# Kernel optimization log

Measured on AMD Instinct MI355X. Metric: run time of the kernel, lower is better.

## Reference

```python
import jax, jax.numpy as jnp
import numpy as np

IN_DIM, UNITS, OUT_DIM = 128, 256, 8
DENSITY = 0.5  # 1 - sparsity_level
B, T = 256, 512


def _ncp_dims():
    Nm = OUT_DIM
    Nc = max(int(0.4 * (UNITS - Nm)), 1)   # command neurons (AutoNCP rule)
    Ni = UNITS - Nm - Nc                    # inter neurons
    return Ni, Nc, Nm


def _fanout_mask(rng, n_src, n_dst, fanout):
    # each source connects to `fanout` distinct random destinations
    idx = np.argsort(rng.random((n_src, n_dst)), axis=1)[:, :fanout]
    m = np.zeros((n_src, n_dst), dtype=np.int32)
    m[np.arange(n_src)[:, None], idx] = 1
    return m


def setup_inputs() -> dict:
    key = jax.random.key(0)
    rng = np.random.default_rng(22222)
    Ni, Nc, Nm = _ncp_dims()
    s_fan = max(int(Ni * DENSITY), 1)       # sensory fanout
    i_fan = max(int(Nc * DENSITY), 1)       # inter fanout
    m_fanin = max(int(Nc * DENSITY), 1)     # motor fanin
    M_si = _fanout_mask(rng, IN_DIM, Ni, s_fan)      # sensory -> inter
    M_ic = _fanout_mask(rng, Ni, Nc, i_fan)          # inter -> command
    M_cm = _fanout_mask(rng, Nm, Nc, m_fanin).T      # command -> motor (fanin per motor)

    def layer_mask(M_in, hid):
        # WiredCfCCell: concat input sparsity with dense ones for the recurrent block, then transpose
        return np.concatenate([M_in, np.ones((hid, hid), np.int32)], axis=0).T

    masks = [layer_mask(M_si, Ni), layer_mask(M_ic, Nc), layer_mask(M_cm, Nm)]
    dims = [(IN_DIM, Ni), (Ni, Nc), (Nc, Nm)]
    inp = {}
    for l, (fin, hid) in enumerate(dims):
        cat = fin + hid
        scale = 1.0 / np.sqrt(cat)
        for nm in ("w1", "w2", "wa", "wb"):
            inp[f"{nm}_{l}"] = jnp.asarray(rng.normal(0.0, scale, (hid, cat)).astype(np.float32))
        for nm in ("b1", "b2", "ba", "bb"):
            inp[f"{nm}_{l}"] = jnp.zeros((hid,), jnp.float32)
        inp[f"m{l}"] = jnp.asarray(masks[l])  # int32, constant sparsity mask
    k1, k2 = jax.random.split(key)
    inp["x"] = jax.random.normal(k1, (B, T, IN_DIM), jnp.float32)
    inp["dt"] = jax.random.uniform(k2, (1,), jnp.float32, 0.5, 1.5)
    return inp


def _cfc_cell(xh, w1, b1, w2, b2, wa, ba, wb, bb, m, ts):
    # CfCCell, mode='default', no backbone, sparsity mask on ff1/ff2 weights
    mf = m.astype(w1.dtype)
    ff1 = jnp.tanh(xh @ (w1 * mf).T + b1)
    ff2 = jnp.tanh(xh @ (w2 * mf).T + b2)
    t_interp = jax.nn.sigmoid((xh @ wa.T + ba) * ts + (xh @ wb.T + bb))
    return ff1 * (1.0 - t_interp) + t_interp * ff2


def _forward(x, dt, params, masks):
    Ni, Nc, Nm = _ncp_dims()
    ts = dt[0]
    h0 = jnp.zeros((x.shape[0], Ni), x.dtype)
    h1 = jnp.zeros((x.shape[0], Nc), x.dtype)
    h2 = jnp.zeros((x.shape[0], Nm), x.dtype)
    p0, p1, p2 = params

    def step(carry, xt):
        h0, h1, h2 = carry
        nh0 = _cfc_cell(jnp.concatenate([xt, h0], 1), *p0, masks[0], ts)
        nh1 = _cfc_cell(jnp.concatenate([nh0, h1], 1), *p1, masks[1], ts)
        nh2 = _cfc_cell(jnp.concatenate([nh1, h2], 1), *p2, masks[2], ts)
        return (nh0, nh1, nh2), nh2

    (h0, h1, h2), ys = jax.lax.scan(step, (h0, h1, h2), jnp.swapaxes(x, 0, 1))
    y = jnp.tanh(jnp.swapaxes(ys, 0, 1))          # (B, T, OUT_DIM), tanh output saturation
    h_out = jnp.concatenate([h0, h1, h2], axis=1)  # (B, units)
    return y, h_out


def reference(x, dt,
              w1_0, b1_0, w2_0, b2_0, wa_0, ba_0, wb_0, bb_0, m0,
              w1_1, b1_1, w2_1, b2_1, wa_1, ba_1, wb_1, bb_1, m1,
              w1_2, b1_2, w2_2, b2_2, wa_2, ba_2, wb_2, bb_2, m2):
    params = ((w1_0, b1_0, w2_0, b2_0, wa_0, ba_0, wb_0, bb_0),
              (w1_1, b1_1, w2_1, b2_1, wa_1, ba_1, wb_1, bb_1),
              (w1_2, b1_2, w2_2, b2_2, wa_2, ba_2, wb_2, bb_2))
    return _forward(x, dt, params, (m0, m1, m2))
```

## Files before the change

kernel.cpp:

```cpp
#include <hip/hip_runtime.h>
#include <cmath>


typedef _Float16 f16;
typedef f16 h4 __attribute__((ext_vector_type(4)));
typedef f16 h8 __attribute__((ext_vector_type(8)));
typedef float f4 __attribute__((ext_vector_type(4)));

#define MFMA(a, b, c) __builtin_amdgcn_mfma_f32_16x16x32_f16(a, b, c, 0, 0, 0)
#define RAW_BAR() asm volatile("s_waitcnt lgkmcnt(0)\n\ts_barrier" ::: "memory")

constexpr int IN_DIM = 128, Ni = 149, Nc = 99, Nm = 8;
constexpr int CAT0 = 277, CAT1 = 248, CAT2 = 107;
constexpr int Bsz = 256, Tsz = 512;
constexpr int TC = 64, NCH = 8, NBT = 16;
constexpr int NT0 = 30, NT1 = 21;
constexpr int S0 = 168, S2 = 136;
constexpr int NXWG1 = 64;
constexpr int NXWG0 = 128;
constexpr size_t XU0C = (size_t)TC * NBT * NT0 * 256;
constexpr size_t NH0C = (size_t)TC * NBT * 2560;
constexpr size_t XU1C = (size_t)TC * NBT * NT1 * 256;
constexpr size_t H0S_HALVES = (size_t)NBT * 16 * S0;
constexpr size_t H12S_HALVES = (size_t)NBT * 2 * 16 * S2;
constexpr size_t YOFF = (size_t)Bsz * Tsz * 8;
constexpr float L2E = 1.4426950408889634f;

constexpr int OFF_X0 = 0;
constexpr int OFF_R0 = 7680;
constexpr int OFF_X1 = 17280;
constexpr int OFF_R12A = 24000;
constexpr int OFF_R12B = 29376;
constexpr int NFRAG = 30144;

__device__ inline float rcpf_(float x) { return __builtin_amdgcn_rcpf(x); }
__device__ __forceinline__ float exp2p_(float x) {
#if __has_builtin(__builtin_amdgcn_exp2f)
  return __builtin_amdgcn_exp2f(x);
#else
  return exp2f(x);
#endif
}
__device__ __forceinline__ float cfc_h(float a0, float a1, float a2) {
  float e0 = exp2p_(a0), e1 = exp2p_(a1), e2 = exp2p_(a2);
  float pa = 1.f + e0, ma = 1.f - e0;
  float pb = 1.f + e1, mb = 1.f - e1;
  float pc = 1.f + e2;
  float num = fmaf(ma * pb, e2, mb * pa);
  return num * rcpf_(pa * pb * pc);
}
__device__ __forceinline__ float tanhp_(float x) {
  float e = exp2p_(-2.f * L2E * x);
  return (1.f - e) * rcpf_(1.f + e);
}

__global__ __launch_bounds__(256) void pack_kernel(
    const float* __restrict__ w1_0, const float* __restrict__ w2_0,
    const float* __restrict__ wa_0, const float* __restrict__ wb_0,
    const int* __restrict__ m0,
    const float* __restrict__ w1_1, const float* __restrict__ w2_1,
    const float* __restrict__ wa_1, const float* __restrict__ wb_1,
    const int* __restrict__ m1,
    const float* __restrict__ w1_2, const float* __restrict__ w2_2,
    const float* __restrict__ wa_2, const float* __restrict__ wb_2,
    const int* __restrict__ m2, const float* __restrict__ dtp,
    f16* __restrict__ PK, int* __restrict__ CNT) {
  if (blockIdx.x == 0 && threadIdx.x < NCH)
    __hip_atomic_store(&CNT[threadIdx.x], 0, __ATOMIC_RELAXED,
                       __HIP_MEMORY_SCOPE_AGENT);
  int idx = blockIdx.x * 256 + threadIdx.x;
  if (idx >= NFRAG) return;
  int lane = idx & 63, col = lane & 15, q = lane >> 4;
  float ts = dtp[0];
  const float* Wa = nullptr;
  const float* Wb = nullptr;
  const int* M = nullptr;
  int ld, n, nmax, k0, kmax;
  int mat;
  if (idx < OFF_R0) {
    int p = idx >> 6;
    mat = p / 40; int nt = (p >> 2) % 10, kt = p & 3;
    ld = CAT0; n = nt * 16 + col; nmax = Ni; k0 = kt * 32 + q * 8; kmax = IN_DIM;
    if (mat == 0) { Wa = w1_0; M = m0; }
    else if (mat == 1) { Wa = w2_0; M = m0; }
    else { Wa = wa_0; Wb = wb_0; }
  } else if (idx < OFF_X1) {
    int p = (idx - OFF_R0) >> 6;
    int g = p / 15; mat = (p / 5) % 3; int kt = p % 5;
    ld = CAT0; n = g * 16 + col; nmax = Ni; k0 = IN_DIM + kt * 32 + q * 8; kmax = CAT0;
    if (mat == 0) Wa = w1_0;
    else if (mat == 1) Wa = w2_0;
    else { Wa = wa_0; Wb = wb_0; }
  } else if (idx < OFF_R12A) {
    int p = (idx - OFF_X1) >> 6;
    mat = p / 35; int nt = (p / 5) % 7, kt = p % 5;
    ld = CAT1; n = nt * 16 + col; nmax = Nc; k0 = kt * 32 + q * 8; kmax = Ni;
    if (mat == 0) { Wa = w1_1; M = m1; }
    else if (mat == 1) { Wa = w2_1; M = m1; }
    else { Wa = wa_1; Wb = wb_1; }
  } else if (idx < OFF_R12B) {
    int p = (idx - OFF_R12A) >> 6;
    int wv = p / 12; mat = (p / 4) % 3; int kt = p & 3;
    ld = CAT1; n = wv * 16 + col; nmax = Nc; k0 = Ni + kt * 32 + q * 8; kmax = CAT1;
    if (mat == 0) Wa = w1_1;
    else if (mat == 1) Wa = w2_1;
    else { Wa = wa_1; Wb = wb_1; }
  } else {
    int p = (idx - OFF_R12B) >> 6;
    mat = p / 4; int kt = p & 3;
    ld = CAT2; n = col; nmax = Nm; k0 = kt * 32 + q * 8; kmax = CAT2;
    if (mat == 0) { Wa = w1_2; M = m2; }
    else if (mat == 1) { Wa = w2_2; M = m2; }
    else { Wa = wa_2; Wb = wb_2; }
  }
  h8 r;
#pragma unroll
  for (int j = 0; j < 8; j++) {
    int k = k0 + j;
    float v = 0.f;
    if (n < nmax && k < kmax) {
      if (mat < 2) {
        v = Wa[(size_t)n * ld + k];
        if (M) v *= (float)M[(size_t)n * ld + k];
        v *= -2.f * L2E;
      } else {
        v = -L2E * (ts * Wa[(size_t)n * ld + k] + Wb[(size_t)n * ld + k]);
      }
    }
    r[j] = (f16)v;
  }
  ((h8*)PK)[idx] = r;
}

__device__ __forceinline__ void r0_step(
    const f16* br, f16* bw, const f16* __restrict__ XU0, f16* __restrict__ NH0,
    float* __restrict__ out, const h8 (&Bf)[3][5], h4 (&xu)[3],
    int t, int tload, int bt, int g, int lane, int col, int q, int n, bool last) {
  h8 A[5];
#pragma unroll
  for (int kt = 0; kt < 5; kt++)
    A[kt] = *(const h8*)(br + col * S0 + kt * 32 + q * 8);
  f4 acc0 = {(float)xu[0][0], (float)xu[0][1], (float)xu[0][2], (float)xu[0][3]};
  f4 acc1 = {(float)xu[1][0], (float)xu[1][1], (float)xu[1][2], (float)xu[1][3]};
  f4 acc2 = {(float)xu[2][0], (float)xu[2][1], (float)xu[2][2], (float)xu[2][3]};
  size_t mtl = (size_t)tload * NBT + bt;
#pragma unroll
  for (int mat = 0; mat < 3; mat++)
    xu[mat] = *(const h4*)(XU0 + (mtl * NT0 + mat * 10 + g) * 256 + lane * 4);
#pragma unroll
  for (int kt = 0; kt < 5; kt++) {
    acc0 = MFMA(A[kt], Bf[0][kt], acc0);
    acc1 = MFMA(A[kt], Bf[1][kt], acc1);
    acc2 = MFMA(A[kt], Bf[2][kt], acc2);
  }
  int mt = t * NBT + bt;
  f16* nh = NH0 + (size_t)mt * 2560;
#pragma unroll
  for (int r = 0; r < 4; r++) {
    int m = q * 4 + r;
    float h = cfc_h(acc0[r], acc1[r], acc2[r]);
    f16 h16 = (f16)h;
    bw[m * S0 + n] = h16;
    nh[m * 160 + n] = h16;
    if (last && n < Ni) out[YOFF + (size_t)(bt * 16 + m) * 256 + n] = h;
  }
}

__device__ __forceinline__ void r12l1_step(
    const f16* br, f16* bw, const f16* __restrict__ XU1, float* __restrict__ out,
    const h8 (&Bf)[3][4], h4 (&xu)[3],
    int tload, int bt, int w, int lane, int col, int q, int n, bool last) {
  h8 A[4];
#pragma unroll
  for (int kt = 0; kt < 4; kt++)
    A[kt] = *(const h8*)(br + col * S2 + kt * 32 + q * 8);
  f4 acc0 = {(float)xu[0][0], (float)xu[0][1], (float)xu[0][2], (float)xu[0][3]};
  f4 acc1 = {(float)xu[1][0], (float)xu[1][1], (float)xu[1][2], (float)xu[1][3]};
  f4 acc2 = {(float)xu[2][0], (float)xu[2][1], (float)xu[2][2], (float)xu[2][3]};
  size_t mtl = (size_t)tload * NBT + bt;
#pragma unroll
  for (int mat = 0; mat < 3; mat++)
    xu[mat] = *(const h4*)(XU1 + (mtl * NT1 + mat * 7 + w) * 256 + lane * 4);
#pragma unroll
  for (int kt = 0; kt < 4; kt++) {
    acc0 = MFMA(A[kt], Bf[0][kt], acc0);
    acc1 = MFMA(A[kt], Bf[1][kt], acc1);
    acc2 = MFMA(A[kt], Bf[2][kt], acc2);
  }
#pragma unroll
  for (int r = 0; r < 4; r++) {
    int m = q * 4 + r;
    float h = cfc_h(acc0[r], acc1[r], acc2[r]);
    if (n < Nc) {
      bw[m * S2 + n] = (f16)h;
      if (last) out[YOFF + (size_t)(bt * 16 + m) * 256 + Ni + n] = h;
    }
  }
}

__device__ __forceinline__ void r12l2_step(
    const f16* rb, f16* wb, float* __restrict__ out, const h8 (&Bf)[3][4],
    float bn0, float bn1, float bn2, int tg, int bt, int col, int q, bool last) {
  h8 A[4];
#pragma unroll
  for (int kt = 0; kt < 4; kt++)
    A[kt] = *(const h8*)(rb + col * S2 + kt * 32 + q * 8);
  f4 acc0 = {bn0, bn0, bn0, bn0};
  f4 acc1 = {bn1, bn1, bn1, bn1};
  f4 acc2 = {bn2, bn2, bn2, bn2};
#pragma unroll
  for (int kt = 0; kt < 4; kt++) {
    acc0 = MFMA(A[kt], Bf[0][kt], acc0);
    acc1 = MFMA(A[kt], Bf[1][kt], acc1);
    acc2 = MFMA(A[kt], Bf[2][kt], acc2);
  }
#pragma unroll
  for (int r = 0; r < 4; r++) {
    int m = q * 4 + r;
    float h = cfc_h(acc0[r], acc1[r], acc2[r]);
    if (col < Nm) {
      out[((size_t)(bt * 16 + m) * Tsz + tg) * 8 + col] = tanhp_(h);
      wb[m * S2 + Nc + col] = (f16)h;
      if (last) out[YOFF + (size_t)(bt * 16 + m) * 256 + Ni + Nc + col] = h;
    }
  }
}

__global__ __launch_bounds__(640) void R_kernel(
    const h8* __restrict__ pk,
    const float* __restrict__ b1_0, const float* __restrict__ b2_0,
    const float* __restrict__ ba_0, const float* __restrict__ bb_0,
    const float* __restrict__ b1_1, const float* __restrict__ b2_1,
    const float* __restrict__ ba_1, const float* __restrict__ bb_1,
    const float* __restrict__ c1, const float* __restrict__ c2,
    const float* __restrict__ ca, const float* __restrict__ cb,
    const float* __restrict__ dtp, const float* __restrict__ x,
    f16* __restrict__ XU0, f16* __restrict__ NH0, f16* __restrict__ XU1,
    f16* __restrict__ H0S, f16* __restrict__ H12S,
    int* __restrict__ CNT, float* __restrict__ out, int c) {
  __shared__ __align__(16) char smem[10752];
  int tid = threadIdx.x;
  int g = tid >> 6, lane = tid & 63, col = lane & 15, q = lane >> 4;
  int wg = blockIdx.x;
  float ts = dtp[0];

  if (wg < NBT) {
    if (c < 0 || c >= NCH) return;
    const f16* XU0r = XU0 + (size_t)(c & 1) * XU0C;
    f16* NH0w = NH0 + (size_t)(c & 1) * NH0C;
    f16(*buf)[16 * S0] = (f16(*)[16 * S0])smem;
    int bt = wg;
    int n = g * 16 + col;
    h8 Bf[3][5];
#pragma unroll
    for (int mat = 0; mat < 3; mat++)
#pragma unroll
      for (int kt = 0; kt < 5; kt++)
        Bf[mat][kt] = pk[OFF_R0 + ((g * 3 + mat) * 5 + kt) * 64 + lane];

    for (int idx = tid; idx < 16 * S0; idx += 640) {
      buf[0][idx] = (c == 0) ? (f16)0.f : H0S[(size_t)bt * 16 * S0 + idx];
      buf[1][idx] = (f16)0.f;
    }
    __syncthreads();

    h4 xu0[3], xu1[3], xu2[3], xu3[3];
#pragma unroll
    for (int mat = 0; mat < 3; mat++) {
      xu0[mat] = *(const h4*)(XU0r + ((size_t)(0 * NBT + bt) * NT0 + mat * 10 + g) * 256 + lane * 4);
      xu1[mat] = *(const h4*)(XU0r + ((size_t)(1 * NBT + bt) * NT0 + mat * 10 + g) * 256 + lane * 4);
      xu2[mat] = *(const h4*)(XU0r + ((size_t)(2 * NBT + bt) * NT0 + mat * 10 + g) * 256 + lane * 4);
      xu3[mat] = *(const h4*)(XU0r + ((size_t)(3 * NBT + bt) * NT0 + mat * 10 + g) * 256 + lane * 4);
    }

    for (int t = 0; t < TC; t += 4) {
      r0_step(buf[0], buf[1], XU0r, NH0w, out, Bf, xu0, t, (t + 4 < TC) ? t + 4 : t,
              bt, g, lane, col, q, n, false);
      RAW_BAR();
      r0_step(buf[1], buf[0], XU0r, NH0w, out, Bf, xu1, t + 1,
              (t + 5 < TC) ? t + 5 : t + 1, bt, g, lane, col, q, n, false);
      RAW_BAR();
      r0_step(buf[0], buf[1], XU0r, NH0w, out, Bf, xu2, t + 2,
              (t + 6 < TC) ? t + 6 : t + 2, bt, g, lane, col, q, n, false);
      RAW_BAR();
      bool lastD = (c == NCH - 1) && (t + 3 == TC - 1);
      r0_step(buf[1], buf[0], XU0r, NH0w, out, Bf, xu3, t + 3,
              (t + 7 < TC) ? t + 7 : t + 3, bt, g, lane, col, q, n, lastD);
      RAW_BAR();
    }
    for (int idx = tid; idx < 16 * S0; idx += 640)
      H0S[(size_t)bt * 16 * S0 + idx] = buf[0][idx];

  } else if (wg < 2 * NBT) {
    int cc = c - 1;
    if (cc < 0 || cc >= NCH) return;
    const f16* XU1r = XU1 + (size_t)(cc & 1) * XU1C;
    f16(*buf)[16 * S2] = (f16(*)[16 * S2])smem;
    int bt = wg - NBT;
    int w = g;
    int n = w * 16 + col;
    h8 Bf[3][4];
    float bn0 = 0.f, bn1 = 0.f, bn2 = 0.f;
    if (w < 7) {
#pragma unroll
      for (int mat = 0; mat < 3; mat++)
#pragma unroll
        for (int kt = 0; kt < 4; kt++)
          Bf[mat][kt] = pk[OFF_R12A + ((w * 3 + mat) * 4 + kt) * 64 + lane];
    } else if (w == 7) {
#pragma unroll
      for (int mat = 0; mat < 3; mat++)
#pragma unroll
        for (int kt = 0; kt < 4; kt++)
          Bf[mat][kt] = pk[OFF_R12B + (mat * 4 + kt) * 64 + lane];
      bn0 = (col < Nm) ? -2.f * L2E * c1[col] : 0.f;
      bn1 = (col < Nm) ? -2.f * L2E * c2[col] : 0.f;
      bn2 = (col < Nm) ? -L2E * (ts * ca[col] + cb[col]) : 0.f;
    }
    for (int idx = tid; idx < 2 * 16 * S2; idx += 640)
      ((f16*)buf)[idx] = (cc == 0) ? (f16)0.f : H12S[(size_t)bt * 2 * 16 * S2 + idx];
    __syncthreads();

    if (tid == 0) {
      long it = 0;
      while (__hip_atomic_load(&CNT[cc], __ATOMIC_RELAXED,
                               __HIP_MEMORY_SCOPE_AGENT) < NXWG1 &&
             it < (1L << 28)) {
        __builtin_amdgcn_s_sleep(8);
        ++it;
      }
    }
    __syncthreads();
    __builtin_amdgcn_fence(__ATOMIC_ACQUIRE, "agent");

    h4 xuA[3], xuB[3];
    if (w < 7) {
#pragma unroll
      for (int mat = 0; mat < 3; mat++) {
        xuA[mat] = *(const h4*)(XU1r + ((size_t)bt * NT1 + mat * 7 + w) * 256 + lane * 4);
        xuB[mat] = *(const h4*)(XU1r +
                                ((size_t)(NBT + bt) * NT1 + mat * 7 + w) * 256 + lane * 4);
      }
    }

    for (int t = 0; t < TC; t += 2) {
      if (w < 7) {
        int tlA = (t + 2 < TC) ? t + 2 : t;
        r12l1_step(buf[0], buf[1], XU1r, out, Bf, xuA, tlA, bt, w, lane, col, q, n,
                   false);
      }
      RAW_BAR();
      if (w == 7)
        r12l2_step(buf[1], buf[0], out, Bf, bn0, bn1, bn2, cc * TC + t, bt, col, q,
                   false);
      if (w < 7) {
        int tlB = (t + 3 < TC) ? t + 3 : t + 1;
        bool lastB = (cc == NCH - 1) && (t + 1 == TC - 1);
        r12l1_step(buf[1], buf[0], XU1r, out, Bf, xuB, tlB, bt, w, lane, col, q, n,
                   lastB);
      }
      RAW_BAR();
      if (w == 7)
        r12l2_step(buf[0], buf[1], out, Bf, bn0, bn1, bn2, cc * TC + t + 1, bt, col, q,
                   (cc == NCH - 1) && (t + 1 == TC - 1));
    }
    __syncthreads();
    for (int idx = tid; idx < 2 * 16 * S2; idx += 640)
      H12S[(size_t)bt * 2 * 16 * S2 + idx] = ((f16*)buf)[idx];

  } else if (wg < 2 * NBT + NXWG1) {
    int cx = c - 1;
    if (cx < 0 || cx >= NCH) return;
    int w = g;
    const f16* NH0r = NH0 + (size_t)(cx & 1) * NH0C;
    f16* XU1w = XU1 + (size_t)(cx & 1) * XU1C;
    int bx = wg - 2 * NBT;
    int n = w * 16 + col;
    if (w < 7) {
      h8 Bf[3][5];
      float bias[3];
#pragma unroll
      for (int mat = 0; mat < 3; mat++)
#pragma unroll
        for (int kt = 0; kt < 5; kt++)
          Bf[mat][kt] = pk[OFF_X1 + (mat * 35 + w * 5 + kt) * 64 + lane];
      bias[0] = (n < Nc) ? -2.f * L2E * b1_1[n] : 0.f;
      bias[1] = (n < Nc) ? -2.f * L2E * b2_1[n] : 0.f;
      bias[2] = (n < Nc) ? -L2E * (ts * ba_1[n] + bb_1[n]) : 0.f;
      for (int i = 0; i < (TC * NBT) / NXWG1; i++) {
        int mt = bx * ((TC * NBT) / NXWG1) + i;
        const f16* Ab = NH0r + (size_t)mt * 2560;
        h8 A[5];
#pragma unroll
        for (int kt = 0; kt < 5; kt++)
          A[kt] = *(const h8*)(Ab + col * 160 + kt * 32 + q * 8);
#pragma unroll
        for (int mat = 0; mat < 3; mat++) {
          float b = bias[mat];
          f4 acc = {b, b, b, b};
#pragma unroll
          for (int kt = 0; kt < 5; kt++) acc = MFMA(A[kt], Bf[mat][kt], acc);
          h4 o;
#pragma unroll
          for (int rr = 0; rr < 4; rr++) o[rr] = (f16)acc[rr];
          *(h4*)(XU1w + ((size_t)mt * NT1 + mat * 7 + w) * 256 + lane * 4) = o;
        }
      }
    }
    __syncthreads();
    if (tid == 0)
      __hip_atomic_fetch_add(&CNT[cx], 1, __ATOMIC_RELEASE,
                             __HIP_MEMORY_SCOPE_AGENT);

  } else {
    int cn = c + 1;
    if (cn >= NCH) return;
    f16* XU0w = XU0 + (size_t)(cn & 1) * XU0C;
    f16* stg = (f16*)smem;
    int bx = wg - 2 * NBT - NXWG1;
    int w = g;
    int n = w * 16 + col;
    h8 Bx[3][4];
    float bias[3];
#pragma unroll
    for (int mat = 0; mat < 3; mat++)
#pragma unroll
      for (int kt = 0; kt < 4; kt++)
        Bx[mat][kt] = pk[OFF_X0 + ((mat * 10 + w) * 4 + kt) * 64 + lane];
    bias[0] = (n < Ni) ? -2.f * L2E * b1_0[n] : 0.f;
    bias[1] = (n < Ni) ? -2.f * L2E * b2_0[n] : 0.f;
    bias[2] = (n < Ni) ? -L2E * (ts * ba_0[n] + bb_0[n]) : 0.f;
    for (int i = 0; i < (TC * NBT) / NXWG0; i++) {
      int mt = bx * ((TC * NBT) / NXWG0) + i;
      int tl = mt >> 4, bt = mt & 15;
      int tg = cn * TC + tl;
      if (tid < 256) {
        int sr = tid >> 4, sc = (tid & 15) * 8;
        const float* xp = x + ((size_t)(bt * 16 + sr) * Tsz + tg) * IN_DIM + sc;
        h8 hv;
#pragma unroll
        for (int j = 0; j < 8; j++) hv[j] = (f16)xp[j];
        *(h8*)(stg + sr * 136 + sc) = hv;
      }
      __syncthreads();
      h8 A[4];
#pragma unroll
      for (int kt = 0; kt < 4; kt++)
        A[kt] = *(const h8*)(stg + col * 136 + kt * 32 + q * 8);
#pragma unroll
      for (int mat = 0; mat < 3; mat++) {
        float b = bias[mat];
        f4 acc = {b, b, b, b};
#pragma unroll
        for (int kt = 0; kt < 4; kt++) acc = MFMA(A[kt], Bx[mat][kt], acc);
        h4 o;
#pragma unroll
        for (int rr = 0; rr < 4; rr++) o[rr] = (f16)acc[rr];
        *(h4*)(XU0w + ((size_t)mt * NT0 + mat * 10 + w) * 256 + lane * 4) = o;
      }
      __syncthreads();
    }
  }
}

extern "C" void kernel_launch(void* const* d_in, const int* in_sizes, int n_in,
                              void* d_out, int out_size, void* d_ws, size_t ws_size,
                              hipStream_t stream) {
  const float* w1_0 = (const float*)d_in[0];
  const float* w2_0 = (const float*)d_in[1];
  const float* wa_0 = (const float*)d_in[2];
  const float* wb_0 = (const float*)d_in[3];
  const float* b1_0 = (const float*)d_in[4];
  const float* b2_0 = (const float*)d_in[5];
  const float* ba_0 = (const float*)d_in[6];
  const float* bb_0 = (const float*)d_in[7];
  const int* m0 = (const int*)d_in[8];
  const float* w1_1 = (const float*)d_in[9];
  const float* w2_1 = (const float*)d_in[10];
  const float* wa_1 = (const float*)d_in[11];
  const float* wb_1 = (const float*)d_in[12];
  const float* b1_1 = (const float*)d_in[13];
  const float* b2_1 = (const float*)d_in[14];
  const float* ba_1 = (const float*)d_in[15];
  const float* bb_1 = (const float*)d_in[16];
  const int* m1 = (const int*)d_in[17];
  const float* w1_2 = (const float*)d_in[18];
  const float* w2_2 = (const float*)d_in[19];
  const float* wa_2 = (const float*)d_in[20];
  const float* wb_2 = (const float*)d_in[21];
  const float* c1 = (const float*)d_in[22];
  const float* c2 = (const float*)d_in[23];
  const float* ca = (const float*)d_in[24];
  const float* cb = (const float*)d_in[25];
  const int* m2 = (const int*)d_in[26];
  const float* x = (const float*)d_in[27];
  const float* dt = (const float*)d_in[28];
  float* out = (float*)d_out;

  f16* XU0 = (f16*)d_ws;
  f16* NH0 = XU0 + 2 * XU0C;
  f16* XU1 = NH0 + 2 * NH0C;
  f16* H0S = XU1 + 2 * XU1C;
  f16* H12S = H0S + H0S_HALVES;
  f16* PK = H12S + H12S_HALVES;
  int* CNT = (int*)(PK + (size_t)NFRAG * 8);
  const h8* pk = (const h8*)PK;

  pack_kernel<<<(NFRAG + 255) / 256, 256, 0, stream>>>(
      w1_0, w2_0, wa_0, wb_0, m0, w1_1, w2_1, wa_1, wb_1, m1,
      w1_2, w2_2, wa_2, wb_2, m2, dt, PK, CNT);

  for (int c = -1; c <= NCH; c++)
    R_kernel<<<2 * NBT + NXWG1 + NXWG0, 640, 0, stream>>>(
        pk, b1_0, b2_0, ba_0, bb_0, b1_1, b2_1, ba_1, bb_1,
        c1, c2, ca, cb, dt, x, XU0, NH0, XU1, H0S, H12S, CNT, out, c);
}
```

Baseline: 732.8 us.

## Fuse chunked launches into one persistent kernel with per-chunk counter flags

Replaces the ten per-chunk launches of R_kernel with a single persistent launch in which each role (x-projection, layer-0 recurrence, layer-1 projection, layers-1/2 recurrence) loops over all chunks and synchronises through per-chunk atomic counters padded to separate cache lines. Because recurrent state now stays in LDS across chunks, the H0S/H12S state spill and reload between launches is removed. This removes launch gaps and the implicit grid-wide barrier between stages, letting stages of different chunks overlap. The trade-off is a reliance on all 240 workgroups being co-resident, since spin-waits could otherwise deadlock (bounded only by an iteration cap), and added polling overhead.

```diff
diff --git a/kernel.cpp b/kernel.cpp
--- a/kernel.cpp
+++ b/kernel.cpp
@@ -21,8 +21,6 @@
 constexpr size_t XU0C = (size_t)TC * NBT * NT0 * 256;
 constexpr size_t NH0C = (size_t)TC * NBT * 2560;
 constexpr size_t XU1C = (size_t)TC * NBT * NT1 * 256;
-constexpr size_t H0S_HALVES = (size_t)NBT * 16 * S0;
-constexpr size_t H12S_HALVES = (size_t)NBT * 2 * 16 * S2;
 constexpr size_t YOFF = (size_t)Bsz * Tsz * 8;
 constexpr float L2E = 1.4426950408889634f;
 
@@ -32,6 +30,10 @@
 constexpr int OFF_R12A = 24000;
 constexpr int OFF_R12B = 29376;
 constexpr int NFRAG = 30144;
+
+constexpr int CSTRIDE = 16;
+constexpr int C_X0 = 0, C_R0 = 8, C_X1 = 16, C_R12 = 24;
+constexpr int NCNT = 32 * CSTRIDE;
 
 __device__ inline float rcpf_(float x) { return __builtin_amdgcn_rcpf(x); }
 __device__ __forceinline__ float exp2p_(float x) {
@@ -52,6 +54,26 @@
 __device__ __forceinline__ float tanhp_(float x) {
   float e = exp2p_(-2.f * L2E * x);
   return (1.f - e) * rcpf_(1.f + e);
+}
+
+__device__ __forceinline__ void spin_ge(int* p, int target) {
+  if (threadIdx.x == 0) {
+    if (__hip_atomic_load(p, __ATOMIC_RELAXED, __HIP_MEMORY_SCOPE_AGENT) < target) {
+      long it = 0;
+      do {
+        __builtin_amdgcn_s_sleep(4);
+      } while (__hip_atomic_load(p, __ATOMIC_RELAXED, __HIP_MEMORY_SCOPE_AGENT) <
+                   target &&
+               ++it < (1L << 22));
+    }
+  }
+  __syncthreads();
+  __builtin_amdgcn_fence(__ATOMIC_ACQUIRE, "agent");
+}
+__device__ __forceinline__ void signal(int* p) {
+  __syncthreads();
+  if (threadIdx.x == 0)
+    __hip_atomic_fetch_add(p, 1, __ATOMIC_RELEASE, __HIP_MEMORY_SCOPE_AGENT);
 }
 
 __global__ __launch_bounds__(256) void pack_kernel(
@@ -65,9 +87,9 @@
     const float* __restrict__ wa_2, const float* __restrict__ wb_2,
     const int* __restrict__ m2, const float* __restrict__ dtp,
     f16* __restrict__ PK, int* __restrict__ CNT) {
-  if (blockIdx.x == 0 && threadIdx.x < NCH)
-    __hip_atomic_store(&CNT[threadIdx.x], 0, __ATOMIC_RELAXED,
-                       __HIP_MEMORY_SCOPE_AGENT);
+  if (blockIdx.x == 0)
+    for (int i = threadIdx.x; i < NCNT; i += 256)
+      __hip_atomic_store(&CNT[i], 0, __ATOMIC_RELAXED, __HIP_MEMORY_SCOPE_AGENT);
   int idx = blockIdx.x * 256 + threadIdx.x;
   if (idx >= NFRAG) return;
   int lane = idx & 63, col = lane & 15, q = lane >> 4;
@@ -236,8 +258,7 @@
     const float* __restrict__ ca, const float* __restrict__ cb,
     const float* __restrict__ dtp, const float* __restrict__ x,
     f16* __restrict__ XU0, f16* __restrict__ NH0, f16* __restrict__ XU1,
-    f16* __restrict__ H0S, f16* __restrict__ H12S,
-    int* __restrict__ CNT, float* __restrict__ out, int c) {
+    int* __restrict__ CNT, float* __restrict__ out) {
   __shared__ __align__(16) char smem[10752];
   int tid = threadIdx.x;
   int g = tid >> 6, lane = tid & 63, col = lane & 15, q = lane >> 4;
@@ -245,9 +266,6 @@
   float ts = dtp[0];
 
   if (wg < NBT) {
-    if (c < 0 || c >= NCH) return;
-    const f16* XU0r = XU0 + (size_t)(c & 1) * XU0C;
-    f16* NH0w = NH0 + (size_t)(c & 1) * NH0C;
     f16(*buf)[16 * S0] = (f16(*)[16 * S0])smem;
     int bt = wg;
     int n = g * 16 + col;
@@ -257,44 +275,41 @@
 #pragma unroll
       for (int kt = 0; kt < 5; kt++)
         Bf[mat][kt] = pk[OFF_R0 + ((g * 3 + mat) * 5 + kt) * 64 + lane];
-
-    for (int idx = tid; idx < 16 * S0; idx += 640) {
-      buf[0][idx] = (c == 0) ? (f16)0.f : H0S[(size_t)bt * 16 * S0 + idx];
-      buf[1][idx] = (f16)0.f;
-    }
+    for (int idx = tid; idx < 2 * 16 * S0; idx += 640) ((f16*)buf)[idx] = (f16)0.f;
     __syncthreads();
 
-    h4 xu0[3], xu1[3], xu2[3], xu3[3];
-#pragma unroll
-    for (int mat = 0; mat < 3; mat++) {
-      xu0[mat] = *(const h4*)(XU0r + ((size_t)(0 * NBT + bt) * NT0 + mat * 10 + g) * 256 + lane * 4);
-      xu1[mat] = *(const h4*)(XU0r + ((size_t)(1 * NBT + bt) * NT0 + mat * 10 + g) * 256 + lane * 4);
-      xu2[mat] = *(const h4*)(XU0r + ((size_t)(2 * NBT + bt) * NT0 + mat * 10 + g) * 256 + lane * 4);
-      xu3[mat] = *(const h4*)(XU0r + ((size_t)(3 * NBT + bt) * NT0 + mat * 10 + g) * 256 + lane * 4);
-    }
-
-    for (int t = 0; t < TC; t += 4) {
-      r0_step(buf[0], buf[1], XU0r, NH0w, out, Bf, xu0, t, (t + 4 < TC) ? t + 4 : t,
-              bt, g, lane, col, q, n, false);
-      RAW_BAR();
-      r0_step(buf[1], buf[0], XU0r, NH0w, out, Bf, xu1, t + 1,
-              (t + 5 < TC) ? t + 5 : t + 1, bt, g, lane, col, q, n, false);
-      RAW_BAR();
-      r0_step(buf[0], buf[1], XU0r, NH0w, out, Bf, xu2, t + 2,
-              (t + 6 < TC) ? t + 6 : t + 2, bt, g, lane, col, q, n, false);
-      RAW_BAR();
-      bool lastD = (c == NCH - 1) && (t + 3 == TC - 1);
-      r0_step(buf[1], buf[0], XU0r, NH0w, out, Bf, xu3, t + 3,
-              (t + 7 < TC) ? t + 7 : t + 3, bt, g, lane, col, q, n, lastD);
-      RAW_BAR();
-    }
-    for (int idx = tid; idx < 16 * S0; idx += 640)
-      H0S[(size_t)bt * 16 * S0 + idx] = buf[0][idx];
+    for (int c = 0; c < NCH; ++c) {
+      spin_ge(&CNT[(C_X0 + c) * CSTRIDE], NXWG0);
+      if (c >= 2) spin_ge(&CNT[(C_X1 + c - 2) * CSTRIDE], NXWG1);
+      const f16* XU0r = XU0 + (size_t)(c & 1) * XU0C;
+      f16* NH0w = NH0 + (size_t)(c & 1) * NH0C;
+      h4 xu0[3], xu1[3], xu2[3], xu3[3];
+#pragma unroll
+      for (int mat = 0; mat < 3; mat++) {
+        xu0[mat] = *(const h4*)(XU0r + ((size_t)(0 * NBT + bt) * NT0 + mat * 10 + g) * 256 + lane * 4);
+        xu1[mat] = *(const h4*)(XU0r + ((size_t)(1 * NBT + bt) * NT0 + mat * 10 + g) * 256 + lane * 4);
+        xu2[mat] = *(const h4*)(XU0r + ((size_t)(2 * NBT + bt) * NT0 + mat * 10 + g) * 256 + lane * 4);
+        xu3[mat] = *(const h4*)(XU0r + ((size_t)(3 * NBT + bt) * NT0 + mat * 10 + g) * 256 + lane * 4);
+      }
+      for (int t = 0; t < TC; t += 4) {
+        r0_step(buf[0], buf[1], XU0r, NH0w, out, Bf, xu0, t, (t + 4 < TC) ? t + 4 : t,
+                bt, g, lane, col, q, n, false);
+        RAW_BAR();
+        r0_step(buf[1], buf[0], XU0r, NH0w, out, Bf, xu1, t + 1,
+                (t + 5 < TC) ? t + 5 : t + 1, bt, g, lane, col, q, n, false);
+        RAW_BAR();
+        r0_step(buf[0], buf[1], XU0r, NH0w, out, Bf, xu2, t + 2,
+                (t + 6 < TC) ? t + 6 : t + 2, bt, g, lane, col, q, n, false);
+        RAW_BAR();
+        bool lastD = (c == NCH - 1) && (t + 3 == TC - 1);
+        r0_step(buf[1], buf[0], XU0r, NH0w, out, Bf, xu3, t + 3,
+                (t + 7 < TC) ? t + 7 : t + 3, bt, g, lane, col, q, n, lastD);
+        RAW_BAR();
+      }
+      signal(&CNT[(C_R0 + c) * CSTRIDE]);
+    }
 
   } else if (wg < 2 * NBT) {
-    int cc = c - 1;
-    if (cc < 0 || cc >= NCH) return;
-    const f16* XU1r = XU1 + (size_t)(cc & 1) * XU1C;
     f16(*buf)[16 * S2] = (f16(*)[16 * S2])smem;
     int bt = wg - NBT;
     int w = g;
@@ -317,68 +332,52 @@
       bn1 = (col < Nm) ? -2.f * L2E * c2[col] : 0.f;
       bn2 = (col < Nm) ? -L2E * (ts * ca[col] + cb[col]) : 0.f;
     }
-    for (int idx = tid; idx < 2 * 16 * S2; idx += 640)
-      ((f16*)buf)[idx] = (cc == 0) ? (f16)0.f : H12S[(size_t)bt * 2 * 16 * S2 + idx];
+    for (int idx = tid; idx < 2 * 16 * S2; idx += 640) ((f16*)buf)[idx] = (f16)0.f;
     __syncthreads();
 
-    if (tid == 0) {
-      long it = 0;
-      while (__hip_atomic_load(&CNT[cc], __ATOMIC_RELAXED,
-                               __HIP_MEMORY_SCOPE_AGENT) < NXWG1 &&
-             it < (1L << 28)) {
-        __builtin_amdgcn_s_sleep(8);
-        ++it;
-      }
-    }
-    __syncthreads();
-    __builtin_amdgcn_fence(__ATOMIC_ACQUIRE, "agent");
-
-    h4 xuA[3], xuB[3];
+    for (int cc = 0; cc < NCH; ++cc) {
+      spin_ge(&CNT[(C_X1 + cc) * CSTRIDE], NXWG1);
+      const f16* XU1r = XU1 + (size_t)(cc & 1) * XU1C;
+      h4 xuA[3], xuB[3];
+      if (w < 7) {
+#pragma unroll
+        for (int mat = 0; mat < 3; mat++) {
+          xuA[mat] = *(const h4*)(XU1r + ((size_t)bt * NT1 + mat * 7 + w) * 256 + lane * 4);
+          xuB[mat] = *(const h4*)(XU1r +
+                                  ((size_t)(NBT + bt) * NT1 + mat * 7 + w) * 256 + lane * 4);
+        }
+      }
+      for (int t = 0; t < TC; t += 2) {
+        if (w < 7) {
+          int tlA = (t + 2 < TC) ? t + 2 : t;
+          r12l1_step(buf[0], buf[1], XU1r, out, Bf, xuA, tlA, bt, w, lane, col, q, n,
+                     false);
+        }
+        RAW_BAR();
+        if (w == 7)
+          r12l2_step(buf[1], buf[0], out, Bf, bn0, bn1, bn2, cc * TC + t, bt, col, q,
+                     false);
+        if (w < 7) {
+          int tlB = (t + 3 < TC) ? t + 3 : t + 1;
+          bool lastB = (cc == NCH - 1) && (t + 1 == TC - 1);
+          r12l1_step(buf[1], buf[0], XU1r, out, Bf, xuB, tlB, bt, w, lane, col, q, n,
+                     lastB);
+        }
+        RAW_BAR();
+        if (w == 7)
+          r12l2_step(buf[0], buf[1], out, Bf, bn0, bn1, bn2, cc * TC + t + 1, bt, col,
+                     q, (cc == NCH - 1) && (t + 1 == TC - 1));
+      }
+      signal(&CNT[(C_R12 + cc) * CSTRIDE]);
+    }
+
+  } else if (wg < 2 * NBT + NXWG1) {
+    int bx = wg - 2 * NBT;
+    int w = g;
+    int n = w * 16 + col;
+    h8 Bf[3][5];
+    float bias[3] = {0.f, 0.f, 0.f};
     if (w < 7) {
-#pragma unroll
-      for (int mat = 0; mat < 3; mat++) {
-        xuA[mat] = *(const h4*)(XU1r + ((size_t)bt * NT1 + mat * 7 + w) * 256 + lane * 4);
-        xuB[mat] = *(const h4*)(XU1r +
-                                ((size_t)(NBT + bt) * NT1 + mat * 7 + w) * 256 + lane * 4);
-      }
-    }
-
-    for (int t = 0; t < TC; t += 2) {
-      if (w < 7) {
-        int tlA = (t + 2 < TC) ? t + 2 : t;
-        r12l1_step(buf[0], buf[1], XU1r, out, Bf, xuA, tlA, bt, w, lane, col, q, n,
-                   false);
-      }
-      RAW_BAR();
-      if (w == 7)
-        r12l2_step(buf[1], buf[0], out, Bf, bn0, bn1, bn2, cc * TC + t, bt, col, q,
-                   false);
-      if (w < 7) {
-        int tlB = (t + 3 < TC) ? t + 3 : t + 1;
-        bool lastB = (cc == NCH - 1) && (t + 1 == TC - 1);
-        r12l1_step(buf[1], buf[0], XU1r, out, Bf, xuB, tlB, bt, w, lane, col, q, n,
-                   lastB);
-      }
-      RAW_BAR();
-      if (w == 7)
-        r12l2_step(buf[0], buf[1], out, Bf, bn0, bn1, bn2, cc * TC + t + 1, bt, col, q,
-                   (cc == NCH - 1) && (t + 1 == TC - 1));
-    }
-    __syncthreads();
-    for (int idx = tid; idx < 2 * 16 * S2; idx += 640)
-      H12S[(size_t)bt * 2 * 16 * S2 + idx] = ((f16*)buf)[idx];
-
-  } else if (wg < 2 * NBT + NXWG1) {
-    int cx = c - 1;
-    if (cx < 0 || cx >= NCH) return;
-    int w = g;
-    const f16* NH0r = NH0 + (size_t)(cx & 1) * NH0C;
-    f16* XU1w = XU1 + (size_t)(cx & 1) * XU1C;
-    int bx = wg - 2 * NBT;
-    int n = w * 16 + col;
-    if (w < 7) {
-      h8 Bf[3][5];
-      float bias[3];
 #pragma unroll
       for (int mat = 0; mat < 3; mat++)
 #pragma unroll
@@ -387,35 +386,37 @@
       bias[0] = (n < Nc) ? -2.f * L2E * b1_1[n] : 0.f;
       bias[1] = (n < Nc) ? -2.f * L2E * b2_1[n] : 0.f;
       bias[2] = (n < Nc) ? -L2E * (ts * ba_1[n] + bb_1[n]) : 0.f;
-      for (int i = 0; i < (TC * NBT) / NXWG1; i++) {
-        int mt = bx * ((TC * NBT) / NXWG1) + i;
-        const f16* Ab = NH0r + (size_t)mt * 2560;
-        h8 A[5];
-#pragma unroll
-        for (int kt = 0; kt < 5; kt++)
-          A[kt] = *(const h8*)(Ab + col * 160 + kt * 32 + q * 8);
-#pragma unroll
-        for (int mat = 0; mat < 3; mat++) {
-          float b = bias[mat];
-          f4 acc = {b, b, b, b};
-#pragma unroll
-          for (int kt = 0; kt < 5; kt++) acc = MFMA(A[kt], Bf[mat][kt], acc);
-          h4 o;
-#pragma unroll
-          for (int rr = 0; rr < 4; rr++) o[rr] = (f16)acc[rr];
-          *(h4*)(XU1w + ((size_t)mt * NT1 + mat * 7 + w) * 256 + lane * 4) = o;
+    }
+    for (int cx = 0; cx < NCH; ++cx) {
+      spin_ge(&CNT[(C_R0 + cx) * CSTRIDE], NBT);
+      if (cx >= 2) spin_ge(&CNT[(C_R12 + cx - 2) * CSTRIDE], NBT);
+      const f16* NH0r = NH0 + (size_t)(cx & 1) * NH0C;
+      f16* XU1w = XU1 + (size_t)(cx & 1) * XU1C;
+      if (w < 7) {
+        for (int i = 0; i < (TC * NBT) / NXWG1; i++) {
+          int mt = bx * ((TC * NBT) / NXWG1) + i;
+          const f16* Ab = NH0r + (size_t)mt * 2560;
+          h8 A[5];
+#pragma unroll
+          for (int kt = 0; kt < 5; kt++)
+            A[kt] = *(const h8*)(Ab + col * 160 + kt * 32 + q * 8);
+#pragma unroll
+          for (int mat = 0; mat < 3; mat++) {
+            float b = bias[mat];
+            f4 acc = {b, b, b, b};
+#pragma unroll
+            for (int kt = 0; kt < 5; kt++) acc = MFMA(A[kt], Bf[mat][kt], acc);
+            h4 o;
+#pragma unroll
+            for (int rr = 0; rr < 4; rr++) o[rr] = (f16)acc[rr];
+            *(h4*)(XU1w + ((size_t)mt * NT1 + mat * 7 + w) * 256 + lane * 4) = o;
+          }
         }
       }
-    }
-    __syncthreads();
-    if (tid == 0)
-      __hip_atomic_fetch_add(&CNT[cx], 1, __ATOMIC_RELEASE,
-                             __HIP_MEMORY_SCOPE_AGENT);
+      signal(&CNT[(C_X1 + cx) * CSTRIDE]);
+    }
 
   } else {
-    int cn = c + 1;
-    if (cn >= NCH) return;
-    f16* XU0w = XU0 + (size_t)(cn & 1) * XU0C;
     f16* stg = (f16*)smem;
     int bx = wg - 2 * NBT - NXWG1;
     int w = g;
@@ -430,35 +431,40 @@
     bias[0] = (n < Ni) ? -2.f * L2E * b1_0[n] : 0.f;
     bias[1] = (n < Ni) ? -2.f * L2E * b2_0[n] : 0.f;
     bias[2] = (n < Ni) ? -L2E * (ts * ba_0[n] + bb_0[n]) : 0.f;
-    for (int i = 0; i < (TC * NBT) / NXWG0; i++) {
-      int mt = bx * ((TC * NBT) / NXWG0) + i;
-      int tl = mt >> 4, bt = mt & 15;
-      int tg = cn * TC + tl;
-      if (tid < 256) {
-        int sr = tid >> 4, sc = (tid & 15) * 8;
-        const float* xp = x + ((size_t)(bt * 16 + sr) * Tsz + tg) * IN_DIM + sc;
-        h8 hv;
-#pragma unroll
-        for (int j = 0; j < 8; j++) hv[j] = (f16)xp[j];
-        *(h8*)(stg + sr * 136 + sc) = hv;
-      }
-      __syncthreads();
-      h8 A[4];
-#pragma unroll
-      for (int kt = 0; kt < 4; kt++)
-        A[kt] = *(const h8*)(stg + col * 136 + kt * 32 + q * 8);
-#pragma unroll
-      for (int mat = 0; mat < 3; mat++) {
-        float b = bias[mat];
-        f4 acc = {b, b, b, b};
-#pragma unroll
-        for (int kt = 0; kt < 4; kt++) acc = MFMA(A[kt], Bx[mat][kt], acc);
-        h4 o;
-#pragma unroll
-        for (int rr = 0; rr < 4; rr++) o[rr] = (f16)acc[rr];
-        *(h4*)(XU0w + ((size_t)mt * NT0 + mat * 10 + w) * 256 + lane * 4) = o;
-      }
-      __syncthreads();
+    for (int cn = 0; cn < NCH; ++cn) {
+      if (cn >= 2) spin_ge(&CNT[(C_R0 + cn - 2) * CSTRIDE], NBT);
+      f16* XU0w = XU0 + (size_t)(cn & 1) * XU0C;
+      for (int i = 0; i < (TC * NBT) / NXWG0; i++) {
+        int mt = bx * ((TC * NBT) / NXWG0) + i;
+        int tl = mt >> 4, bt = mt & 15;
+        int tg = cn * TC + tl;
+        if (tid < 256) {
+          int sr = tid >> 4, sc = (tid & 15) * 8;
+          const float* xp = x + ((size_t)(bt * 16 + sr) * Tsz + tg) * IN_DIM + sc;
+          h8 hv;
+#pragma unroll
+          for (int j = 0; j < 8; j++) hv[j] = (f16)xp[j];
+          *(h8*)(stg + sr * 136 + sc) = hv;
+        }
+        __syncthreads();
+        h8 A[4];
+#pragma unroll
+        for (int kt = 0; kt < 4; kt++)
+          A[kt] = *(const h8*)(stg + col * 136 + kt * 32 + q * 8);
+#pragma unroll
+        for (int mat = 0; mat < 3; mat++) {
+          float b = bias[mat];
+          f4 acc = {b, b, b, b};
+#pragma unroll
+          for (int kt = 0; kt < 4; kt++) acc = MFMA(A[kt], Bx[mat][kt], acc);
+          h4 o;
+#pragma unroll
+          for (int rr = 0; rr < 4; rr++) o[rr] = (f16)acc[rr];
+          *(h4*)(XU0w + ((size_t)mt * NT0 + mat * 10 + w) * 256 + lane * 4) = o;
+        }
+        __syncthreads();
+      }
+      signal(&CNT[(C_X0 + cn) * CSTRIDE]);
     }
   }
 }
@@ -500,18 +506,17 @@
   f16* XU0 = (f16*)d_ws;
   f16* NH0 = XU0 + 2 * XU0C;
   f16* XU1 = NH0 + 2 * NH0C;
-  f16* H0S = XU1 + 2 * XU1C;
-  f16* H12S = H0S + H0S_HALVES;
-  f16* PK = H12S + H12S_HALVES;
+  f16* PK = XU1 + 2 * XU1C;
   int* CNT = (int*)(PK + (size_t)NFRAG * 8);
   const h8* pk = (const h8*)PK;
+
+  hipMemsetAsync(CNT, 0, NCNT * sizeof(int), stream);
 
   pack_kernel<<<(NFRAG + 255) / 256, 256, 0, stream>>>(
       w1_0, w2_0, wa_0, wb_0, m0, w1_1, w2_1, wa_1, wb_1, m1,
       w1_2, w2_2, wa_2, wb_2, m2, dt, PK, CNT);
 
-  for (int c = -1; c <= NCH; c++)
-    R_kernel<<<2 * NBT + NXWG1 + NXWG0, 640, 0, stream>>>(
-        pk, b1_0, b2_0, ba_0, bb_0, b1_1, b2_1, ba_1, bb_1,
-        c1, c2, ca, cb, dt, x, XU0, NH0, XU1, H0S, H12S, CNT, out, c);
-}
+  R_kernel<<<2 * NBT + NXWG1 + NXWG0, 640, 0, stream>>>(
+      pk, b1_0, b2_0, ba_0, bb_0, b1_1, b2_1, ba_1, bb_1,
+      c1, c2, ca, cb, dt, x, XU0, NH0, XU1, CNT, out);
+}
```

Result: slower. 843.0 us (+15.0%).

## Pipeline CfC layers at sub-chunk granularity with fine-grained counter handoffs

Applied to the files above, without the earlier changes.

Splits each 64-step time chunk into four 16-step sub-chunks and adds per-sub-chunk atomic counters. Layer-0 recurrence signals progress after each sub-chunk, and the layer-1 projection and layers 1-2 recurrence start as soon as that sub-chunk is ready instead of waiting a full launch. The aim is shorter pipeline fill/drain bubbles between stages inside each launch. It adds spin-waits, system-coherent stores and loads (sc0 sc1) for the NH0 handoff, and a risk of deadlock if the workgroups are not all co-resident.

```diff
diff --git a/kernel.cpp b/kernel.cpp
--- a/kernel.cpp
+++ b/kernel.cpp
@@ -14,6 +14,7 @@
 constexpr int CAT0 = 277, CAT1 = 248, CAT2 = 107;
 constexpr int Bsz = 256, Tsz = 512;
 constexpr int TC = 64, NCH = 8, NBT = 16;
+constexpr int NSUB = NCH * 4;
 constexpr int NT0 = 30, NT1 = 21;
 constexpr int S0 = 168, S2 = 136;
 constexpr int NXWG1 = 64;
@@ -33,6 +34,10 @@
 constexpr int OFF_R12B = 29376;
 constexpr int NFRAG = 30144;
 
+constexpr int CSTRIDE = 16;
+constexpr int C_X0 = 0, C_R0S = 8, C_X1S = 40, C_R12S = 72;
+constexpr int NCNT = 104 * CSTRIDE;
+
 __device__ inline float rcpf_(float x) { return __builtin_amdgcn_rcpf(x); }
 __device__ __forceinline__ float exp2p_(float x) {
 #if __has_builtin(__builtin_amdgcn_exp2f)
@@ -52,6 +57,52 @@
 __device__ __forceinline__ float tanhp_(float x) {
   float e = exp2p_(-2.f * L2E * x);
   return (1.f - e) * rcpf_(1.f + e);
+}
+
+__device__ __forceinline__ void spin_relaxed(int* p, int target) {
+  if (threadIdx.x == 0) {
+    long it = 0;
+    while (__hip_atomic_load(p, __ATOMIC_RELAXED, __HIP_MEMORY_SCOPE_AGENT) <
+               target &&
+           ++it < (1L << 22))
+      __builtin_amdgcn_s_sleep(4);
+  }
+  __syncthreads();
+}
+__device__ __forceinline__ void spin_acq(int* p, int target) {
+  spin_relaxed(p, target);
+  __builtin_amdgcn_fence(__ATOMIC_ACQUIRE, "agent");
+}
+__device__ __forceinline__ void sig_relaxed(int* p) {
+  __syncthreads();
+  if (threadIdx.x == 0)
+    __hip_atomic_fetch_add(p, 1, __ATOMIC_RELAXED, __HIP_MEMORY_SCOPE_AGENT);
+}
+__device__ __forceinline__ void sig_rel(int* p) {
+  __syncthreads();
+  if (threadIdx.x == 0)
+    __hip_atomic_fetch_add(p, 1, __ATOMIC_RELEASE, __HIP_MEMORY_SCOPE_AGENT);
+}
+
+__device__ __forceinline__ void store_short_sc(f16* p, f16 v) {
+  unsigned u = (unsigned)__builtin_bit_cast(unsigned short, v);
+  asm volatile("global_store_short %0, %1, off sc0 sc1" ::"v"(
+                   (unsigned long long)p),
+               "v"(u)
+               : "memory");
+}
+__device__ __forceinline__ void load_A5_sc(const f16* base, h8 (&A)[5]) {
+  unsigned long long b = (unsigned long long)base;
+  asm volatile(
+      "global_load_dwordx4 %0, %5, off sc0 sc1\n\t"
+      "global_load_dwordx4 %1, %5, off offset:64 sc0 sc1\n\t"
+      "global_load_dwordx4 %2, %5, off offset:128 sc0 sc1\n\t"
+      "global_load_dwordx4 %3, %5, off offset:192 sc0 sc1\n\t"
+      "global_load_dwordx4 %4, %5, off offset:256 sc0 sc1\n\t"
+      "s_waitcnt vmcnt(0)"
+      : "=&v"(A[0]), "=&v"(A[1]), "=&v"(A[2]), "=&v"(A[3]), "=&v"(A[4])
+      : "v"(b)
+      : "memory");
 }
 
 __global__ __launch_bounds__(256) void pack_kernel(
@@ -65,9 +116,9 @@
     const float* __restrict__ wa_2, const float* __restrict__ wb_2,
     const int* __restrict__ m2, const float* __restrict__ dtp,
     f16* __restrict__ PK, int* __restrict__ CNT) {
-  if (blockIdx.x == 0 && threadIdx.x < NCH)
-    __hip_atomic_store(&CNT[threadIdx.x], 0, __ATOMIC_RELAXED,
-                       __HIP_MEMORY_SCOPE_AGENT);
+  if (blockIdx.x == 0)
+    for (int i = threadIdx.x; i < NCNT; i += 256)
+      __hip_atomic_store(&CNT[i], 0, __ATOMIC_RELAXED, __HIP_MEMORY_SCOPE_AGENT);
   int idx = blockIdx.x * 256 + threadIdx.x;
   if (idx >= NFRAG) return;
   int lane = idx & 63, col = lane & 15, q = lane >> 4;
@@ -161,7 +212,7 @@
     float h = cfc_h(acc0[r], acc1[r], acc2[r]);
     f16 h16 = (f16)h;
     bw[m * S0 + n] = h16;
-    nh[m * 160 + n] = h16;
+    store_short_sc(nh + (size_t)m * 160 + n, h16);
     if (last && n < Ni) out[YOFF + (size_t)(bt * 16 + m) * 256 + n] = h;
   }
 }
@@ -246,6 +297,9 @@
 
   if (wg < NBT) {
     if (c < 0 || c >= NCH) return;
+    spin_relaxed(&CNT[(C_X0 + c) * CSTRIDE], NXWG0);
+    if (c >= 2)
+      spin_relaxed(&CNT[(C_X1S + 4 * (c - 2) + 3) * CSTRIDE], NBT);
     const f16* XU0r = XU0 + (size_t)(c & 1) * XU0C;
     f16* NH0w = NH0 + (size_t)(c & 1) * NH0C;
     f16(*buf)[16 * S0] = (f16(*)[16 * S0])smem;
@@ -287,14 +341,16 @@
       r0_step(buf[1], buf[0], XU0r, NH0w, out, Bf, xu3, t + 3,
               (t + 7 < TC) ? t + 7 : t + 3, bt, g, lane, col, q, n, lastD);
       RAW_BAR();
+      if ((t & 12) == 12)
+        sig_relaxed(&CNT[(C_R0S + 4 * c + (t >> 4)) * CSTRIDE]);
     }
     for (int idx = tid; idx < 16 * S0; idx += 640)
       H0S[(size_t)bt * 16 * S0 + idx] = buf[0][idx];
 
   } else if (wg < 2 * NBT) {
-    int cc = c - 1;
-    if (cc < 0 || cc >= NCH) return;
-    const f16* XU1r = XU1 + (size_t)(cc & 1) * XU1C;
+    int Glo = 4 * c - 2; if (Glo < 0) Glo = 0;
+    int Ghi = 4 * c + 1; if (Ghi > NSUB - 1) Ghi = NSUB - 1;
+    if (Glo > Ghi || c < 0) return;
     f16(*buf)[16 * S2] = (f16(*)[16 * S2])smem;
     int bt = wg - NBT;
     int w = g;
@@ -318,67 +374,59 @@
       bn2 = (col < Nm) ? -L2E * (ts * ca[col] + cb[col]) : 0.f;
     }
     for (int idx = tid; idx < 2 * 16 * S2; idx += 640)
-      ((f16*)buf)[idx] = (cc == 0) ? (f16)0.f : H12S[(size_t)bt * 2 * 16 * S2 + idx];
+      ((f16*)buf)[idx] = (Glo == 0) ? (f16)0.f : H12S[(size_t)bt * 2 * 16 * S2 + idx];
     __syncthreads();
 
-    if (tid == 0) {
-      long it = 0;
-      while (__hip_atomic_load(&CNT[cc], __ATOMIC_RELAXED,
-                               __HIP_MEMORY_SCOPE_AGENT) < NXWG1 &&
-             it < (1L << 28)) {
-        __builtin_amdgcn_s_sleep(8);
-        ++it;
+    for (int G = Glo; G <= Ghi; ++G) {
+      int m = G >> 2, t0 = (G & 3) * 16;
+      spin_acq(&CNT[(C_X1S + G) * CSTRIDE], NBT);
+      const f16* XU1r = XU1 + (size_t)(m & 1) * XU1C;
+      h4 xuA[3], xuB[3];
+      if (w < 7) {
+#pragma unroll
+        for (int mat = 0; mat < 3; mat++) {
+          xuA[mat] = *(const h4*)(XU1r + ((size_t)(t0 * NBT + bt) * NT1 + mat * 7 + w) * 256 + lane * 4);
+          xuB[mat] = *(const h4*)(XU1r +
+                                  ((size_t)((t0 + 1) * NBT + bt) * NT1 + mat * 7 + w) * 256 + lane * 4);
+        }
       }
-    }
-    __syncthreads();
-    __builtin_amdgcn_fence(__ATOMIC_ACQUIRE, "agent");
-
-    h4 xuA[3], xuB[3];
-    if (w < 7) {
-#pragma unroll
-      for (int mat = 0; mat < 3; mat++) {
-        xuA[mat] = *(const h4*)(XU1r + ((size_t)bt * NT1 + mat * 7 + w) * 256 + lane * 4);
-        xuB[mat] = *(const h4*)(XU1r +
-                                ((size_t)(NBT + bt) * NT1 + mat * 7 + w) * 256 + lane * 4);
+      for (int t = t0; t < t0 + 16; t += 2) {
+        if (w < 7) {
+          int tlA = (t + 2 < t0 + 16) ? t + 2 : t;
+          r12l1_step(buf[0], buf[1], XU1r, out, Bf, xuA, tlA, bt, w, lane, col, q, n,
+                     false);
+        }
+        RAW_BAR();
+        if (w == 7)
+          r12l2_step(buf[1], buf[0], out, Bf, bn0, bn1, bn2, m * TC + t, bt, col, q,
+                     false);
+        if (w < 7) {
+          int tlB = (t + 3 < t0 + 16) ? t + 3 : t + 1;
+          bool lastB = (m == NCH - 1) && (t + 1 == TC - 1);
+          r12l1_step(buf[1], buf[0], XU1r, out, Bf, xuB, tlB, bt, w, lane, col, q, n,
+                     lastB);
+        }
+        RAW_BAR();
+        if (w == 7)
+          r12l2_step(buf[0], buf[1], out, Bf, bn0, bn1, bn2, m * TC + t + 1, bt, col,
+                     q, (m == NCH - 1) && (t + 1 == TC - 1));
       }
-    }
-
-    for (int t = 0; t < TC; t += 2) {
-      if (w < 7) {
-        int tlA = (t + 2 < TC) ? t + 2 : t;
-        r12l1_step(buf[0], buf[1], XU1r, out, Bf, xuA, tlA, bt, w, lane, col, q, n,
-                   false);
-      }
-      RAW_BAR();
-      if (w == 7)
-        r12l2_step(buf[1], buf[0], out, Bf, bn0, bn1, bn2, cc * TC + t, bt, col, q,
-                   false);
-      if (w < 7) {
-        int tlB = (t + 3 < TC) ? t + 3 : t + 1;
-        bool lastB = (cc == NCH - 1) && (t + 1 == TC - 1);
-        r12l1_step(buf[1], buf[0], XU1r, out, Bf, xuB, tlB, bt, w, lane, col, q, n,
-                   lastB);
-      }
-      RAW_BAR();
-      if (w == 7)
-        r12l2_step(buf[0], buf[1], out, Bf, bn0, bn1, bn2, cc * TC + t + 1, bt, col, q,
-                   (cc == NCH - 1) && (t + 1 == TC - 1));
-    }
-    __syncthreads();
+      sig_relaxed(&CNT[(C_R12S + G) * CSTRIDE]);
+    }
     for (int idx = tid; idx < 2 * 16 * S2; idx += 640)
       H12S[(size_t)bt * 2 * 16 * S2 + idx] = ((f16*)buf)[idx];
 
   } else if (wg < 2 * NBT + NXWG1) {
-    int cx = c - 1;
-    if (cx < 0 || cx >= NCH) return;
+    int bx = wg - 2 * NBT;
+    int k = bx >> 4;
+    int m = (k == 3) ? c - 1 : c;
+    if (m < 0 || m >= NCH) return;
+    int G = 4 * m + k;
     int w = g;
-    const f16* NH0r = NH0 + (size_t)(cx & 1) * NH0C;
-    f16* XU1w = XU1 + (size_t)(cx & 1) * XU1C;
-    int bx = wg - 2 * NBT;
     int n = w * 16 + col;
+    h8 Bf[3][5];
+    float bias[3] = {0.f, 0.f, 0.f};
     if (w < 7) {
-      h8 Bf[3][5];
-      float bias[3];
 #pragma unroll
       for (int mat = 0; mat < 3; mat++)
 #pragma unroll
@@ -387,13 +435,18 @@
       bias[0] = (n < Nc) ? -2.f * L2E * b1_1[n] : 0.f;
       bias[1] = (n < Nc) ? -2.f * L2E * b2_1[n] : 0.f;
       bias[2] = (n < Nc) ? -L2E * (ts * ba_1[n] + bb_1[n]) : 0.f;
-      for (int i = 0; i < (TC * NBT) / NXWG1; i++) {
-        int mt = bx * ((TC * NBT) / NXWG1) + i;
-        const f16* Ab = NH0r + (size_t)mt * 2560;
+    }
+    spin_relaxed(&CNT[(C_R0S + G) * CSTRIDE], NBT);
+    if (m >= 2)
+      spin_relaxed(&CNT[(C_R12S + 4 * (m - 2) + 3) * CSTRIDE], NBT);
+    const f16* NH0r = NH0 + (size_t)(m & 1) * NH0C;
+    f16* XU1w = XU1 + (size_t)(m & 1) * XU1C;
+    if (w < 7) {
+      for (int i = 0; i < 16; i++) {
+        int mt = bx * 16 + i;
+        const f16* base = NH0r + (size_t)mt * 2560 + col * 160 + q * 8;
         h8 A[5];
-#pragma unroll
-        for (int kt = 0; kt < 5; kt++)
-          A[kt] = *(const h8*)(Ab + col * 160 + kt * 32 + q * 8);
+        load_A5_sc(base, A);
 #pragma unroll
         for (int mat = 0; mat < 3; mat++) {
           float b = bias[mat];
@@ -407,14 +460,13 @@
         }
       }
     }
-    __syncthreads();
-    if (tid == 0)
-      __hip_atomic_fetch_add(&CNT[cx], 1, __ATOMIC_RELEASE,
-                             __HIP_MEMORY_SCOPE_AGENT);
+    sig_rel(&CNT[(C_X1S + G) * CSTRIDE]);
 
   } else {
     int cn = c + 1;
     if (cn >= NCH) return;
+    if (cn >= 2)
+      spin_relaxed(&CNT[(C_R0S + 4 * (cn - 2) + 3) * CSTRIDE], NBT);
     f16* XU0w = XU0 + (size_t)(cn & 1) * XU0C;
     f16* stg = (f16*)smem;
     int bx = wg - 2 * NBT - NXWG1;
@@ -460,6 +512,7 @@
       }
       __syncthreads();
     }
+    sig_relaxed(&CNT[(C_X0 + cn) * CSTRIDE]);
   }
 }
 
@@ -506,6 +559,8 @@
   int* CNT = (int*)(PK + (size_t)NFRAG * 8);
   const h8* pk = (const h8*)PK;
 
+  hipMemsetAsync(CNT, 0, NCNT * sizeof(int), stream);
+
   pack_kernel<<<(NFRAG + 255) / 256, 256, 0, stream>>>(
       w1_0, w2_0, wa_0, wb_0, m0, w1_1, w2_1, wa_1, wb_1, m1,
       w1_2, w2_2, wa_2, wb_2, m2, dt, PK, CNT);
```

Result: faster. 706.0 us (-3.7%).
